# Optimization experiments

Hardware: AMD Instinct MI355X
Metric: run time of the kernel (lower is better)

Reference implementation:

```python
import jax, jax.numpy as jnp
import numpy as np

T, B, D_POSE, H, K_CODES = 30, 1024, 135, 512, 512
EPS = 1e-5


def _bn_relu(x, g, b):
    # BatchNorm1d (training-mode batch stats, biased var) + ReLU; x: (B, C, L)
    m = x.mean(axis=(0, 2), keepdims=True)
    v = x.var(axis=(0, 2), keepdims=True)
    y = g[None, :, None] * (x - m) * jax.lax.rsqrt(v + EPS) + b[None, :, None]
    return jax.nn.relu(y)


def _conv_sk(x, w):
    # Conv1d with stride == kernel_size (non-overlapping): pure reshaped GEMM.
    # x: (B, I, L), w: (O, I, K) torch layout -> (B, O, L//K)
    Bn, I, L = x.shape
    O, _, K = w.shape
    xr = x.reshape(Bn, I, L // K, K)
    return jnp.einsum('bitk,oik->bot', xr, w)


def _convT_sk(x, w):
    # ConvTranspose1d with stride == kernel_size: x (B, I, L), w (I, O, K) torch layout
    Bn, I, L = x.shape
    _, O, K = w.shape
    return jnp.einsum('bil,iok->bolk', x, w).reshape(Bn, O, L * K)


def setup_inputs() -> dict:
    key = jax.random.key(0)
    ks = jax.random.split(key, 12)
    sc = 0.05
    inp = {
        'input_seqs': jax.random.normal(ks[0], (T, B, D_POSE), jnp.float32),
        'W_in': jax.random.normal(ks[1], (D_POSE, H), jnp.float32) * sc,
        'b_in': jnp.zeros((H,), jnp.float32),
        'w_e1': jax.random.normal(ks[2], (H, H, 5), jnp.float32) * sc,
        'g_e1': jnp.ones((H,), jnp.float32), 'b_e1': jnp.zeros((H,), jnp.float32),
        'w_e2': jax.random.normal(ks[3], (H, H, 3), jnp.float32) * sc,
        'g_e2': jnp.ones((H,), jnp.float32), 'b_e2': jnp.zeros((H,), jnp.float32),
        'w_e3': jax.random.normal(ks[4], (H, H, 2), jnp.float32) * sc,
        'g_e3': jnp.ones((H,), jnp.float32), 'b_e3': jnp.zeros((H,), jnp.float32),
        'codebook': jax.random.normal(ks[5], (K_CODES, H), jnp.float32) * sc,
        'W_q': jax.random.normal(ks[6], (H, H), jnp.float32) * sc,
        'b_q': jnp.zeros((H,), jnp.float32),
        'w_d1': jax.random.normal(ks[7], (H, H, 2), jnp.float32) * sc,
        'g_d1': jnp.ones((H,), jnp.float32), 'b_d1': jnp.zeros((H,), jnp.float32),
        'w_d2': jax.random.normal(ks[8], (H, H, 3), jnp.float32) * sc,
        'g_d2': jnp.ones((H,), jnp.float32), 'b_d2': jnp.zeros((H,), jnp.float32),
        'w_d3': jax.random.normal(ks[9], (H, H, 5), jnp.float32) * sc,
        'g_d3': jnp.ones((H,), jnp.float32), 'b_d3': jnp.zeros((H,), jnp.float32),
        'W_out': jax.random.normal(ks[10], (H, D_POSE), jnp.float32) * sc,
        'b_out': jnp.zeros((D_POSE,), jnp.float32),
    }
    return inp


def reference(input_seqs, W_in, b_in, w_e1, g_e1, b_e1, w_e2, g_e2, b_e2,
              w_e3, g_e3, b_e3, codebook, W_q, b_q,
              w_d1, g_d1, b_d1, w_d2, g_d2, b_d2, w_d3, g_d3, b_d3,
              W_out, b_out):
    commitment_cost = 0.25
    # ---- EncoderCNN ----
    h = input_seqs @ W_in + b_in              # (T, B, H)
    h = jnp.transpose(h, (1, 2, 0))           # (B, H, T)
    h = _bn_relu(_conv_sk(h, w_e1), g_e1, b_e1)   # (B, H, 6)
    h = _bn_relu(_conv_sk(h, w_e2), g_e2, b_e2)   # (B, H, 2)
    z = _bn_relu(_conv_sk(h, w_e3), g_e3, b_e3)   # (B, H, 1)

    # ---- VQ (VQ_Payam, straight-through) ----
    Bn, D, L = z.shape
    flat = jnp.transpose(z, (0, 2, 1)).reshape(-1, D)            # (B*L, D)
    dist = (jnp.sum(flat ** 2, axis=1, keepdims=True)
            + jnp.sum(codebook ** 2, axis=1)
            - 2.0 * flat @ codebook.T)                           # (B*L, K)
    idx = jnp.argmin(dist, axis=1)                               # (B*L,)
    quantized = codebook[idx]                                    # (B*L, D)
    e_latent_loss = jnp.mean((jax.lax.stop_gradient(quantized) - flat) ** 2)
    q_latent_loss = jnp.mean((quantized - jax.lax.stop_gradient(flat)) ** 2)
    vq_loss = q_latent_loss + commitment_cost * e_latent_loss
    q_st = flat + jax.lax.stop_gradient(quantized - flat)        # straight-through
    avg_probs = jnp.mean(jax.nn.one_hot(idx, K_CODES, dtype=flat.dtype), axis=0)
    perplexity = jnp.exp(-jnp.sum(avg_probs * jnp.log(avg_probs + 1e-10)))

    # ---- DecoderCNN ----
    d = q_st @ W_q + b_q                      # (B, H)
    d = d[:, :, None]                         # (B, H, 1)
    d = _bn_relu(_convT_sk(d, w_d1), g_d1, b_d1)  # (B, H, 2)
    d = _bn_relu(_convT_sk(d, w_d2), g_d2, b_d2)  # (B, H, 6)
    d = _bn_relu(_convT_sk(d, w_d3), g_d3, b_d3)  # (B, H, 30)
    recon = jnp.transpose(d, (0, 2, 1)) @ W_out + b_out           # (B, T, D_POSE)
    return recon, vq_loss, perplexity
```

## Files before the change

### kernel.cpp

```cpp
#include <hip/hip_runtime.h>
#include <math.h>


typedef __attribute__((ext_vector_type(8))) short bf16x8;
typedef __attribute__((ext_vector_type(4))) float f32x4;

__device__ __forceinline__ unsigned pk_bf16(float a, float b) {
    unsigned ua = __float_as_uint(a), ub = __float_as_uint(b);
    ua += 0x7fffu + ((ua >> 16) & 1u);
    ub += 0x7fffu + ((ub >> 16) & 1u);
    return (ua >> 16) | (ub & 0xffff0000u);
}
__device__ __forceinline__ unsigned short bfh(float x) {
    unsigned u = __float_as_uint(x);
    u += 0x7fffu + ((u >> 16) & 1u);
    return (unsigned short)(u >> 16);
}
__device__ __forceinline__ float bf2f(unsigned short h) {
    return __uint_as_float(((unsigned)h) << 16);
}

template <int NV>
__device__ __forceinline__ void bn_on_raw(uint4* raw, int kbase,
                                          const float* __restrict__ bnS,
                                          const float* __restrict__ bnB) {
#pragma unroll
    for (int i = 0; i < NV; ++i) {
        unsigned* u4 = (unsigned*)&raw[i];
#pragma unroll
        for (int j = 0; j < 4; ++j) {
            const int k = kbase + (i << 3) + (j << 1);
            unsigned u = u4[j];
            float x0 = __uint_as_float(u << 16);
            float x1 = __uint_as_float(u & 0xffff0000u);
            x0 = fmaxf(fmaf(x0, bnS[k],     bnB[k]),     0.f);
            x1 = fmaxf(fmaf(x1, bnS[k + 1], bnB[k + 1]), 0.f);
            u4[j] = pk_bf16(x0, x1);
        }
    }
}

__device__ __forceinline__ void bn4(float4& a, const float* __restrict__ s,
                                    const float* __restrict__ c) {
    float4 sv = *(const float4*)s;
    float4 cv = *(const float4*)c;
    a.x = fmaxf(fmaf(a.x, sv.x, cv.x), 0.f);
    a.y = fmaxf(fmaf(a.y, sv.y, cv.y), 0.f);
    a.z = fmaxf(fmaf(a.z, sv.z, cv.z), 0.f);
    a.w = fmaxf(fmaf(a.w, sv.w, cv.w), 0.f);
}

#define FBK  32
#define FSTR 36

__global__ __launch_bounds__(256)
void k_gemm(const float* __restrict__ Abase,
            const float* __restrict__ Wt,
            float* __restrict__ Cout,
            const float* __restrict__ bnS, const float* __restrict__ bnB,
            unsigned long long* __restrict__ amin,
            const float* __restrict__ codesq,
            int Mslice, int K, int N, int decK)
{
    __shared__ __align__(16) float As[FBK][FSTR];
    __shared__ __align__(16) float Bs[FBK][FSTR];

    const int tid = threadIdx.x;
    const int z  = blockIdx.z;
    const int n0 = blockIdx.x << 5;
    const int m0 = blockIdx.y << 5;
    const int ty = tid >> 4;
    const int tx = tid & 15;

    const int a_slice = z / decK, wk = z - a_slice * decK;
    const float* Ap = Abase + (size_t)a_slice * (size_t)Mslice * (size_t)K;
    const float* Wp = Wt    + (size_t)wk * (size_t)K * (size_t)N;

    const int sr  = tid >> 3;
    const int sc4 = (tid & 7) << 2;

    int mrow = m0 + sr;
    if (mrow > Mslice - 1) mrow = Mslice - 1;
    const float* Arow_p = Ap + (size_t)mrow * K;

    float acc[2][2];
    acc[0][0] = 0.f; acc[0][1] = 0.f; acc[1][0] = 0.f; acc[1][1] = 0.f;

    float4 pa = *(const float4*)(Arow_p + sc4);
    if (bnS != nullptr) bn4(pa, bnS + sc4, bnB + sc4);
    float4 pb = *(const float4*)(Wp + (size_t)sr * N + n0 + sc4);

    for (int k0 = 0; k0 < K; k0 += FBK) {
        __syncthreads();
        As[sc4 + 0][sr] = pa.x;
        As[sc4 + 1][sr] = pa.y;
        As[sc4 + 2][sr] = pa.z;
        As[sc4 + 3][sr] = pa.w;
        *(float4*)&Bs[sr][sc4] = pb;
        const int k0n = k0 + FBK;
        if (k0n < K) {
            pa = *(const float4*)(Arow_p + k0n + sc4);
            if (bnS != nullptr) bn4(pa, bnS + k0n + sc4, bnB + k0n + sc4);
            pb = *(const float4*)(Wp + (size_t)(k0n + sr) * N + n0 + sc4);
        }
        __syncthreads();
#pragma unroll
        for (int kk = 0; kk < FBK; ++kk) {
            float2 av = *(const float2*)&As[kk][ty << 1];
            float2 bv = *(const float2*)&Bs[kk][tx << 1];
            acc[0][0] = fmaf(av.x, bv.x, acc[0][0]);
            acc[0][1] = fmaf(av.x, bv.y, acc[0][1]);
            acc[1][0] = fmaf(av.y, bv.x, acc[1][0]);
            acc[1][1] = fmaf(av.y, bv.y, acc[1][1]);
        }
    }

    if (amin != nullptr) {
        float2 cq = *(const float2*)(codesq + n0 + (tx << 1));
#pragma unroll
        for (int i = 0; i < 2; ++i) {
            const int m = m0 + (ty << 1) + i;
            float d0 = cq.x - 2.f * acc[i][0];
            float d1 = cq.y - 2.f * acc[i][1];
            int bj = (d1 < d0) ? 1 : 0;
            float best = (d1 < d0) ? d1 : d0;
            unsigned u = __float_as_uint(best);
            u = (u & 0x80000000u) ? ~u : (u | 0x80000000u);
            unsigned long long key =
                ((unsigned long long)u << 32) | (unsigned)(n0 + (tx << 1) + bj);
#pragma unroll
            for (int off = 1; off < 16; off <<= 1) {
                unsigned long long o = __shfl_xor(key, off, 64);
                if (o < key) key = o;
            }
            if (tx == 0 && m < Mslice) atomicMin(&amin[m], key);
        }
        return;
    }

#pragma unroll
    for (int i = 0; i < 2; ++i) {
        const int m = m0 + (ty << 1) + i;
        if (m < Mslice) {
            float2 v = make_float2(acc[i][0], acc[i][1]);
            *(float2*)&Cout[((size_t)z * Mslice + m) * N + n0 + (tx << 1)] = v;
        }
    }
}

#define ASTR 72

__global__ __launch_bounds__(256)
void k_mfma_b(const unsigned short* __restrict__ Abase,
              const unsigned short* __restrict__ Bt,
              unsigned short* __restrict__ Cb,
              float* __restrict__ operm,
              const float* __restrict__ bias,
              const float* __restrict__ bnS, const float* __restrict__ bnB,
              float* __restrict__ stats,
              int Mslice, int K, int N, int decK)
{
    __shared__ __align__(16) unsigned short As[128 * ASTR];
    __shared__ __align__(16) unsigned short Bs[128 * ASTR];
    __shared__ float colsum[128], colsq[128];

    const int tid  = threadIdx.x;
    const int lane = tid & 63;
    const int wave = tid >> 6;
    const int wm = (wave >> 1) << 6;
    const int wn = (wave & 1) << 6;
    const int z  = blockIdx.z;
    const int n0 = blockIdx.x << 7;
    const int m0 = blockIdx.y << 7;

    if (stats != nullptr && tid < 128) { colsum[tid] = 0.f; colsq[tid] = 0.f; }

    const int a_slice = z / decK, wk = z - a_slice * decK;
    const unsigned short* Ap = Abase + (size_t)a_slice * (size_t)Mslice * (size_t)K;
    const unsigned short* Bp = Bt + (size_t)wk * (size_t)N * (size_t)K;

    const int sr = tid >> 1;
    const int sk = (tid & 1) << 5;

    const unsigned short* Arow = Ap + (size_t)(m0 + sr) * K + sk;
    const unsigned short* Brow = Bp + (size_t)(n0 + sr) * K + sk;
    const bool bvalid = (n0 + sr) < N;

    f32x4 acc[4][4];
#pragma unroll
    for (int i = 0; i < 4; ++i)
#pragma unroll
        for (int j = 0; j < 4; ++j) acc[i][j] = (f32x4){0.f, 0.f, 0.f, 0.f};

    const int lidx = lane & 15;
    const int lq   = lane >> 4;

    uint4 pa[4], pb[4];
#pragma unroll
    for (int i = 0; i < 4; ++i) pa[i] = *(const uint4*)(Arow + (i << 3));
    if (bnS != nullptr) bn_on_raw<4>(pa, sk, bnS, bnB);
    if (bvalid) {
#pragma unroll
        for (int i = 0; i < 4; ++i) pb[i] = *(const uint4*)(Brow + (i << 3));
    } else {
#pragma unroll
        for (int i = 0; i < 4; ++i) pb[i] = make_uint4(0u, 0u, 0u, 0u);
    }

    for (int k0 = 0; k0 < K; k0 += 64) {
        __syncthreads();
        {
            uint4* dA = (uint4*)&As[sr * ASTR + sk];
            uint4* dB = (uint4*)&Bs[sr * ASTR + sk];
#pragma unroll
            for (int i = 0; i < 4; ++i) { dA[i] = pa[i]; dB[i] = pb[i]; }
        }
        const int k0n = k0 + 64;
        if (k0n < K) {
#pragma unroll
            for (int i = 0; i < 4; ++i) pa[i] = *(const uint4*)(Arow + k0n + (i << 3));
            if (bnS != nullptr) bn_on_raw<4>(pa, k0n + sk, bnS, bnB);
            if (bvalid) {
#pragma unroll
                for (int i = 0; i < 4; ++i) pb[i] = *(const uint4*)(Brow + k0n + (i << 3));
            }
        }
        __syncthreads();
#pragma unroll
        for (int ks = 0; ks < 2; ++ks) {
            const int kb = (ks << 5) + (lq << 3);
            bf16x8 af[4], bfv[4];
#pragma unroll
            for (int t = 0; t < 4; ++t)
                af[t] = *(const bf16x8*)&As[(wm + (t << 4) + lidx) * ASTR + kb];
#pragma unroll
            for (int t = 0; t < 4; ++t)
                bfv[t] = *(const bf16x8*)&Bs[(wn + (t << 4) + lidx) * ASTR + kb];
#pragma unroll
            for (int mt = 0; mt < 4; ++mt)
#pragma unroll
                for (int nt = 0; nt < 4; ++nt)
                    acc[mt][nt] = __builtin_amdgcn_mfma_f32_16x16x32_bf16(
                        af[mt], bfv[nt], acc[mt][nt], 0, 0, 0);
        }
    }

    const int rbase = lq << 2;
#pragma unroll
    for (int nt = 0; nt < 4; ++nt) {
        const int col = n0 + wn + (nt << 4) + lidx;
        const float badd = (bias != nullptr && col < N) ? bias[col] : 0.f;
        float s = 0.f, q = 0.f;
#pragma unroll
        for (int mt = 0; mt < 4; ++mt) {
#pragma unroll
            for (int r = 0; r < 4; ++r) {
                float x = acc[mt][nt][r];
                s += x; q += x * x;
                const int row = m0 + wm + (mt << 4) + rbase + r;
                if (operm != nullptr) {
                    if (col < N) {
                        const int t = row >> 10, b = row & 1023;
                        operm[(size_t)b * 4050 + t * 135 + col] = x + badd;
                    }
                } else {
                    Cb[((size_t)z * Mslice + row) * (size_t)N + col] = bfh(x + badd);
                }
            }
        }
        if (stats != nullptr) {
            s += __shfl_xor(s, 16, 64); s += __shfl_xor(s, 32, 64);
            q += __shfl_xor(q, 16, 64); q += __shfl_xor(q, 32, 64);
            if (lq == 0) {
                atomicAdd(&colsum[wn + (nt << 4) + lidx], s);
                atomicAdd(&colsq [wn + (nt << 4) + lidx], q);
            }
        }
    }
    if (stats != nullptr) {
        __syncthreads();
        if (tid < 128) {
            atomicAdd(&stats[n0 + tid],       colsum[tid]);
            atomicAdd(&stats[512 + n0 + tid], colsq[tid]);
        }
    }
}

#define BSTR 72

__global__ __launch_bounds__(256)
void k_b64(const unsigned short* __restrict__ Abase,
           const unsigned short* __restrict__ Bt,
           unsigned short* __restrict__ Cb,
           const float* __restrict__ bias,
           const float* __restrict__ bnS, const float* __restrict__ bnB,
           float* __restrict__ stats,
           int Mslice, int K, int N, int decK)
{
    __shared__ __align__(16) unsigned short As[64 * BSTR];
    __shared__ __align__(16) unsigned short Bs[64 * BSTR];
    __shared__ float colsum[64], colsq[64];

    const int tid  = threadIdx.x;
    const int lane = tid & 63;
    const int wave = tid >> 6;
    const int wm = (wave >> 1) << 5;
    const int wn = (wave & 1) << 5;
    const int z  = blockIdx.z;
    const int n0 = blockIdx.x << 6;
    const int m0 = blockIdx.y << 6;

    if (stats != nullptr && tid < 64) { colsum[tid] = 0.f; colsq[tid] = 0.f; }

    const int a_slice = z / decK, wk = z - a_slice * decK;
    const unsigned short* Ap = Abase + (size_t)a_slice * (size_t)Mslice * (size_t)K;
    const unsigned short* Bp = Bt + (size_t)wk * (size_t)N * (size_t)K;

    const int sr = tid >> 2;
    const int sk = (tid & 3) << 4;

    const unsigned short* Arow = Ap + (size_t)(m0 + sr) * K + sk;
    const unsigned short* Brow = Bp + (size_t)(n0 + sr) * K + sk;

    f32x4 acc[2][2];
#pragma unroll
    for (int i = 0; i < 2; ++i)
#pragma unroll
        for (int j = 0; j < 2; ++j) acc[i][j] = (f32x4){0.f, 0.f, 0.f, 0.f};

    const int lidx = lane & 15;
    const int lq   = lane >> 4;

    uint4 pa[2], pb[2];
    pa[0] = *(const uint4*)(Arow);
    pa[1] = *(const uint4*)(Arow + 8);
    if (bnS != nullptr) bn_on_raw<2>(pa, sk, bnS, bnB);
    pb[0] = *(const uint4*)(Brow);
    pb[1] = *(const uint4*)(Brow + 8);

    for (int k0 = 0; k0 < K; k0 += 64) {
        __syncthreads();
        {
            uint4* dA = (uint4*)&As[sr * BSTR + sk];
            uint4* dB = (uint4*)&Bs[sr * BSTR + sk];
            dA[0] = pa[0]; dA[1] = pa[1];
            dB[0] = pb[0]; dB[1] = pb[1];
        }
        const int k0n = k0 + 64;
        if (k0n < K) {
            pa[0] = *(const uint4*)(Arow + k0n);
            pa[1] = *(const uint4*)(Arow + k0n + 8);
            if (bnS != nullptr) bn_on_raw<2>(pa, k0n + sk, bnS, bnB);
            pb[0] = *(const uint4*)(Brow + k0n);
            pb[1] = *(const uint4*)(Brow + k0n + 8);
        }
        __syncthreads();
#pragma unroll
        for (int ks = 0; ks < 2; ++ks) {
            const int kb = (ks << 5) + (lq << 3);
            bf16x8 af[2], bfv[2];
#pragma unroll
            for (int t = 0; t < 2; ++t)
                af[t] = *(const bf16x8*)&As[(wm + (t << 4) + lidx) * BSTR + kb];
#pragma unroll
            for (int t = 0; t < 2; ++t)
                bfv[t] = *(const bf16x8*)&Bs[(wn + (t << 4) + lidx) * BSTR + kb];
#pragma unroll
            for (int mt = 0; mt < 2; ++mt)
#pragma unroll
                for (int nt = 0; nt < 2; ++nt)
                    acc[mt][nt] = __builtin_amdgcn_mfma_f32_16x16x32_bf16(
                        af[mt], bfv[nt], acc[mt][nt], 0, 0, 0);
        }
    }

    const int rbase = lq << 2;
#pragma unroll
    for (int nt = 0; nt < 2; ++nt) {
        const int col = n0 + wn + (nt << 4) + lidx;
        const float badd = (bias != nullptr) ? bias[col] : 0.f;
        float s = 0.f, q = 0.f;
#pragma unroll
        for (int mt = 0; mt < 2; ++mt) {
#pragma unroll
            for (int r = 0; r < 4; ++r) {
                float x = acc[mt][nt][r];
                s += x; q += x * x;
                const int row = m0 + wm + (mt << 4) + rbase + r;
                Cb[((size_t)z * Mslice + row) * (size_t)N + col] = bfh(x + badd);
            }
        }
        if (stats != nullptr) {
            s += __shfl_xor(s, 16, 64); s += __shfl_xor(s, 32, 64);
            q += __shfl_xor(q, 16, 64); q += __shfl_xor(q, 32, 64);
            if (lq == 0) {
                atomicAdd(&colsum[wn + (nt << 4) + lidx], s);
                atomicAdd(&colsq [wn + (nt << 4) + lidx], q);
            }
        }
    }
    if (stats != nullptr) {
        __syncthreads();
        if (tid < 64) {
            atomicAdd(&stats[n0 + tid],       colsum[tid]);
            atomicAdd(&stats[512 + n0 + tid], colsq[tid]);
        }
    }
}

#define S64 40

__global__ __launch_bounds__(256)
void k_sp64(const unsigned short* __restrict__ Ahg,
            const unsigned short* __restrict__ Alg,
            const unsigned short* __restrict__ Whi,
            const unsigned short* __restrict__ Wlo,
            float* __restrict__ Cout, float* __restrict__ stats,
            int Mslice, int Kp, int N, int n_terms)
{
    __shared__ __align__(16) unsigned short Ah[64 * S64];
    __shared__ __align__(16) unsigned short Al[64 * S64];
    __shared__ __align__(16) unsigned short Bh[64 * S64];
    __shared__ __align__(16) unsigned short Bl[64 * S64];
    __shared__ float colsum[64], colsq[64];

    const int tid  = threadIdx.x;
    const int lane = tid & 63;
    const int wave = tid >> 6;
    const int wm = (wave >> 1) << 5;
    const int wn = (wave & 1) << 5;
    const int z  = blockIdx.z;
    const int n0 = blockIdx.x << 6;
    const int m0 = blockIdx.y << 6;

    if (stats != nullptr && tid < 64) { colsum[tid] = 0.f; colsq[tid] = 0.f; }

    const int sr = tid >> 2;
    const int sk = (tid & 3) << 3;

    f32x4 acc[2][2];
#pragma unroll
    for (int i = 0; i < 2; ++i)
#pragma unroll
        for (int j = 0; j < 2; ++j) acc[i][j] = (f32x4){0.f, 0.f, 0.f, 0.f};

    const int lidx = lane & 15;
    const int lq   = lane >> 4;
    const int kb   = lq << 3;

    const int cpk = Kp >> 5;
    const int tot = n_terms * cpk;

    uint4 rah, ral, rbh, rblv;
    {
        const size_t ab = ((size_t)(z * n_terms) * Mslice + m0 + sr) * (size_t)Kp + sk;
        rah = *(const uint4*)(Ahg + ab);
        ral = *(const uint4*)(Alg + ab);
        const size_t bb = ((size_t)(n0 + sr)) * (size_t)Kp + sk;
        rbh = *(const uint4*)(Whi + bb);
        rblv = *(const uint4*)(Wlo + bb);
    }
    int lt = 0, lk = 32;
    if (lk >= Kp) { lk = 0; lt = 1; }

    for (int c = 0; c < tot; ++c) {
        __syncthreads();
        *(uint4*)&Ah[sr * S64 + sk] = rah;
        *(uint4*)&Al[sr * S64 + sk] = ral;
        *(uint4*)&Bh[sr * S64 + sk] = rbh;
        *(uint4*)&Bl[sr * S64 + sk] = rblv;
        if (c + 1 < tot) {
            const size_t ab = ((size_t)(z * n_terms + lt) * Mslice + m0 + sr) * (size_t)Kp + lk + sk;
            rah = *(const uint4*)(Ahg + ab);
            ral = *(const uint4*)(Alg + ab);
            const size_t bb = ((size_t)lt * N + n0 + sr) * (size_t)Kp + lk + sk;
            rbh = *(const uint4*)(Whi + bb);
            rblv = *(const uint4*)(Wlo + bb);
            lk += 32; if (lk >= Kp) { lk = 0; ++lt; }
        }
        __syncthreads();
        bf16x8 ah[2], al[2], bh[2], bl[2];
#pragma unroll
        for (int t = 0; t < 2; ++t) {
            const int ra = (wm + (t << 4) + lidx) * S64 + kb;
            ah[t] = *(const bf16x8*)&Ah[ra];
            al[t] = *(const bf16x8*)&Al[ra];
        }
#pragma unroll
        for (int t = 0; t < 2; ++t) {
            const int rb = (wn + (t << 4) + lidx) * S64 + kb;
            bh[t] = *(const bf16x8*)&Bh[rb];
            bl[t] = *(const bf16x8*)&Bl[rb];
        }
#pragma unroll
        for (int mt = 0; mt < 2; ++mt)
#pragma unroll
            for (int nt = 0; nt < 2; ++nt) {
                acc[mt][nt] = __builtin_amdgcn_mfma_f32_16x16x32_bf16(
                    ah[mt], bh[nt], acc[mt][nt], 0, 0, 0);
                acc[mt][nt] = __builtin_amdgcn_mfma_f32_16x16x32_bf16(
                    al[mt], bh[nt], acc[mt][nt], 0, 0, 0);
                acc[mt][nt] = __builtin_amdgcn_mfma_f32_16x16x32_bf16(
                    ah[mt], bl[nt], acc[mt][nt], 0, 0, 0);
            }
    }

    const int rbase = lq << 2;
#pragma unroll
    for (int nt = 0; nt < 2; ++nt) {
        const int col = n0 + wn + (nt << 4) + lidx;
        float s = 0.f, q = 0.f;
#pragma unroll
        for (int mt = 0; mt < 2; ++mt) {
#pragma unroll
            for (int r = 0; r < 4; ++r) {
                float x = acc[mt][nt][r];
                s += x; q += x * x;
                const int row = m0 + wm + (mt << 4) + rbase + r;
                Cout[((size_t)z * Mslice + row) * (size_t)N + col] = x;
            }
        }
        if (stats != nullptr) {
            s += __shfl_xor(s, 16, 64); s += __shfl_xor(s, 32, 64);
            q += __shfl_xor(q, 16, 64); q += __shfl_xor(q, 32, 64);
            if (lq == 0) {
                atomicAdd(&colsum[wn + (nt << 4) + lidx], s);
                atomicAdd(&colsq [wn + (nt << 4) + lidx], q);
            }
        }
    }
    if (stats != nullptr) {
        __syncthreads();
        if (tid < 64) {
            atomicAdd(&stats[n0 + tid],       colsum[tid]);
            atomicAdd(&stats[512 + n0 + tid], colsq[tid]);
        }
    }
}

__global__ void k_prep(float* __restrict__ zbase, unsigned long long* __restrict__ amin,
                       const float* __restrict__ codebook, float* __restrict__ codeT,
                       float* __restrict__ codesq,
                       const float* __restrict__ w_e2, unsigned short* __restrict__ whi_e2,
                       unsigned short* __restrict__ wlo_e2,
                       const float* __restrict__ w_e3, unsigned short* __restrict__ whi_e3,
                       unsigned short* __restrict__ wlo_e3,
                       const float* __restrict__ W_q,  unsigned short* __restrict__ wqb,
                       const float* __restrict__ w_d1, unsigned short* __restrict__ wd1b,
                       const float* __restrict__ w_d2, unsigned short* __restrict__ wd2b,
                       const float* __restrict__ w_d3, unsigned short* __restrict__ wd3b,
                       const float* __restrict__ W_out, unsigned short* __restrict__ woutb,
                       const float* __restrict__ in_seqs,
                       unsigned short* __restrict__ in_h, unsigned short* __restrict__ in_l)
{
    __shared__ float red[4];
    const int bid = blockIdx.x;
    const int tid = threadIdx.x;

    if (bid < 32) {
        int t = bid * 256 + tid;
        if (t < 6720) zbase[t] = 0.f;
        if (t < 1024) amin[t] = ~0ULL;
        return;
    }
    if (bid < 1056) {
        int idx = (bid - 32) * 256 + tid;
        int i = (idx >> 9) & 511, o = idx & 511;
        codeT[idx] = codebook[(o << 9) + i];
        return;
    }
    if (bid < 1568) {
        int c = bid - 1056;
        float s = 0.f;
        for (int i = tid; i < 512; i += 256) { float v = codebook[c * 512 + i]; s += v * v; }
        for (int off = 32; off; off >>= 1) s += __shfl_down(s, off, 64);
        if ((tid & 63) == 0) red[tid >> 6] = s;
        __syncthreads();
        if (tid == 0) codesq[c] = red[0] + red[1] + red[2] + red[3];
        return;
    }
    if (bid < 4640) {
        int idx = (bid - 1568) * 256 + tid;
        int i = idx & 511, o = (idx >> 9) & 511, k = idx >> 18;
        float v = w_e2[(((o << 9) + i) * 3) + k];
        unsigned short h = bfh(v);
        whi_e2[idx] = h; wlo_e2[idx] = bfh(v - bf2f(h));
        return;
    }
    if (bid < 6688) {
        int idx = (bid - 4640) * 256 + tid;
        int i = idx & 511, o = (idx >> 9) & 511, k = idx >> 18;
        float v = w_e3[(((o << 9) + i) * 2) + k];
        unsigned short h = bfh(v);
        whi_e3[idx] = h; wlo_e3[idx] = bfh(v - bf2f(h));
        return;
    }
    if (bid < 7712) {
        int idx = (bid - 6688) * 256 + tid;
        int i = idx & 511, o = (idx >> 9) & 511;
        wqb[idx] = bfh(W_q[((size_t)i << 9) + o]);
        return;
    }
    if (bid < 9760) {
        int idx = (bid - 7712) * 256 + tid;
        int i = idx & 511, o = (idx >> 9) & 511, k = idx >> 18;
        wd1b[idx] = bfh(w_d1[(((size_t)i << 9) + o) * 2 + k]);
        return;
    }
    if (bid < 12832) {
        int idx = (bid - 9760) * 256 + tid;
        int i = idx & 511, o = (idx >> 9) & 511, k = idx >> 18;
        wd2b[idx] = bfh(w_d2[(((size_t)i << 9) + o) * 3 + k]);
        return;
    }
    if (bid < 17952) {
        int idx = (bid - 12832) * 256 + tid;
        int i = idx & 511, o = (idx >> 9) & 511, k = idx >> 18;
        wd3b[idx] = bfh(w_d3[(((size_t)i << 9) + o) * 5 + k]);
        return;
    }
    if (bid < 18222) {
        int idx = (bid - 17952) * 256 + tid;
        if (idx >= 69120) return;
        int i = idx % 512, o = idx / 512;
        woutb[idx] = bfh(W_out[((size_t)i * 135) + o]);
        return;
    }
    {
        int idx = (bid - 18222) * 256 + tid;
        if (idx >= 4915200) return;
        int i = idx % 160, r = idx / 160;
        float v = (i < 135) ? in_seqs[(size_t)r * 135 + i] : 0.f;
        unsigned short h = bfh(v);
        in_h[idx] = h; in_l[idx] = bfh(v - bf2f(h));
    }
}

__global__ void k_repack(const float* __restrict__ w, float* __restrict__ wt,
                         int Kc, int total)
{
    int idx = blockIdx.x * 256 + threadIdx.x;
    if (idx >= total) return;
    int k = idx >> 18;
    int rem = idx & 262143;
    int i = rem >> 9, o = rem & 511;
    wt[idx] = w[(((o << 9) + i) * Kc + k)];
}

__global__ void k_repack_sp_weff(const float* __restrict__ weff,
                                 unsigned short* __restrict__ whi,
                                 unsigned short* __restrict__ wlo,
                                 int total)
{
    int idx = blockIdx.x * 256 + threadIdx.x;
    if (idx >= total) return;
    int i = idx % 160;
    int o = (idx / 160) & 511;
    int t = idx / 81920;
    float v = (i < 135) ? weff[((size_t)t * 135 + i) * 512 + o] : 0.f;
    unsigned short h = bfh(v);
    whi[idx] = h;
    wlo[idx] = bfh(v - bf2f(h));
}

__global__ void k_bnsplit(const float* __restrict__ x,
                          const float* __restrict__ sc, const float* __restrict__ sh,
                          unsigned short* __restrict__ hq, unsigned short* __restrict__ lq_,
                          int total4)
{
    int idx = blockIdx.x * 256 + threadIdx.x;
    if (idx >= total4) return;
    const int base = idx << 2;
    float4 f = *(const float4*)(x + base);
    const int k = base & 511;
    float4 s = *(const float4*)(sc + k);
    float4 c = *(const float4*)(sh + k);
    float y0 = fmaxf(fmaf(f.x, s.x, c.x), 0.f);
    float y1 = fmaxf(fmaf(f.y, s.y, c.y), 0.f);
    float y2 = fmaxf(fmaf(f.z, s.z, c.z), 0.f);
    float y3 = fmaxf(fmaf(f.w, s.w, c.w), 0.f);
    unsigned short h0 = bfh(y0), h1 = bfh(y1), h2 = bfh(y2), h3 = bfh(y3);
    unsigned short l0 = bfh(y0 - bf2f(h0)), l1 = bfh(y1 - bf2f(h1));
    unsigned short l2 = bfh(y2 - bf2f(h2)), l3 = bfh(y3 - bf2f(h3));
    *(uint2*)&hq[base]  = make_uint2((unsigned)h0 | ((unsigned)h1 << 16),
                                     (unsigned)h2 | ((unsigned)h3 << 16));
    *(uint2*)&lq_[base] = make_uint2((unsigned)l0 | ((unsigned)l1 << 16),
                                     (unsigned)l2 | ((unsigned)l3 << 16));
}

__global__ void k_bnapply(const unsigned short* __restrict__ x,
                          const float* __restrict__ sc, const float* __restrict__ sh,
                          unsigned short* __restrict__ y, int total8)
{
    int idx = blockIdx.x * 256 + threadIdx.x;
    if (idx >= total8) return;
    const int base = idx << 3;
    uint4 raw = *(const uint4*)(x + base);
    const int k = base & 511;
    float4 s0 = *(const float4*)(sc + k);
    float4 c0 = *(const float4*)(sh + k);
    float4 s1 = *(const float4*)(sc + k + 4);
    float4 c1 = *(const float4*)(sh + k + 4);
    unsigned* u = (unsigned*)&raw;
    float x0 = __uint_as_float(u[0] << 16),        x1 = __uint_as_float(u[0] & 0xffff0000u);
    float x2 = __uint_as_float(u[1] << 16),        x3 = __uint_as_float(u[1] & 0xffff0000u);
    float x4 = __uint_as_float(u[2] << 16),        x5 = __uint_as_float(u[2] & 0xffff0000u);
    float x6 = __uint_as_float(u[3] << 16),        x7 = __uint_as_float(u[3] & 0xffff0000u);
    x0 = fmaxf(fmaf(x0, s0.x, c0.x), 0.f); x1 = fmaxf(fmaf(x1, s0.y, c0.y), 0.f);
    x2 = fmaxf(fmaf(x2, s0.z, c0.z), 0.f); x3 = fmaxf(fmaf(x3, s0.w, c0.w), 0.f);
    x4 = fmaxf(fmaf(x4, s1.x, c1.x), 0.f); x5 = fmaxf(fmaf(x5, s1.y, c1.y), 0.f);
    x6 = fmaxf(fmaf(x6, s1.z, c1.z), 0.f); x7 = fmaxf(fmaf(x7, s1.w, c1.w), 0.f);
    *(uint4*)&y[base] = make_uint4(pk_bf16(x0, x1), pk_bf16(x2, x3),
                                   pk_bf16(x4, x5), pk_bf16(x6, x7));
}

__global__ void k_bn_fin(const float* __restrict__ stats,
                         const float* __restrict__ g, const float* __restrict__ b,
                         float* __restrict__ sc, float* __restrict__ sh, float inv_n)
{
    int c = blockIdx.x * blockDim.x + threadIdx.x;
    if (c >= 512) return;
    float m = stats[c] * inv_n;
    float v = stats[512 + c] * inv_n - m * m;
    float a = (float)((double)g[c] / sqrt((double)v + 1e-5));
    sc[c] = a;
    sh[c] = b[c] - m * a;
}

__global__ void k_vq_gather(const unsigned long long* __restrict__ amin,
                            const float* __restrict__ codebook,
                            const float* __restrict__ e3pre,
                            const float* __restrict__ sc, const float* __restrict__ sh,
                            unsigned short* __restrict__ quant_bf,
                            float* __restrict__ loss,
                            unsigned int* __restrict__ hist)
{
    int b = blockIdx.x; int t = threadIdx.x;
    unsigned int idx = (unsigned int)(amin[b] & 0xFFFFFFFFull) & 511u;
    float part = 0.f;
    for (int i = t; i < 512; i += 256) {
        float q = codebook[(size_t)idx * 512 + i];
        quant_bf[(size_t)b * 512 + i] = bfh(q);
        float x = e3pre[(size_t)b * 512 + i];
        float f = fmaxf(fmaf(x, sc[i], sh[i]), 0.f);
        float d = q - f;
        part += d * d;
    }
    for (int off = 32; off; off >>= 1) part += __shfl_down(part, off, 64);
    __shared__ float red[4];
    if ((t & 63) == 0) red[t >> 6] = part;
    __syncthreads();
    if (t == 0) {
        atomicAdd(loss, red[0] + red[1] + red[2] + red[3]);
        atomicAdd(&hist[idx], 1u);
    }
}

__global__ void k_scalars(const unsigned int* __restrict__ hist,
                          const float* __restrict__ loss, float* __restrict__ out)
{
    int t = threadIdx.x;
    float p = (float)hist[t] * (1.0f / 1024.0f);
    float e = p * logf(p + 1e-10f);
    for (int off = 32; off; off >>= 1) e += __shfl_down(e, off, 64);
    __shared__ float red[8];
    if ((t & 63) == 0) red[t >> 6] = e;
    __syncthreads();
    if (t == 0) {
        float s = 0.f;
        for (int i = 0; i < 8; ++i) s += red[i];
        out[4147200] = 1.25f * loss[0] * (1.0f / 524288.0f);
        out[4147201] = expf(-s);
    }
}

extern "C" void kernel_launch(void* const* d_in, const int* in_sizes, int n_in,
                              void* d_out, int out_size, void* d_ws, size_t ws_size,
                              hipStream_t stream)
{
    const float* in_seqs = (const float*)d_in[0];
    const float* W_in  = (const float*)d_in[1];
    const float* w_e1  = (const float*)d_in[3];
    const float* g_e1  = (const float*)d_in[4];
    const float* be1   = (const float*)d_in[5];
    const float* w_e2  = (const float*)d_in[6];
    const float* g_e2  = (const float*)d_in[7];
    const float* be2   = (const float*)d_in[8];
    const float* w_e3  = (const float*)d_in[9];
    const float* g_e3  = (const float*)d_in[10];
    const float* be3   = (const float*)d_in[11];
    const float* codebook = (const float*)d_in[12];
    const float* W_q   = (const float*)d_in[13];
    const float* b_q   = (const float*)d_in[14];
    const float* w_d1  = (const float*)d_in[15];
    const float* g_d1  = (const float*)d_in[16];
    const float* bd1   = (const float*)d_in[17];
    const float* w_d2  = (const float*)d_in[18];
    const float* g_d2  = (const float*)d_in[19];
    const float* bd2   = (const float*)d_in[20];
    const float* w_d3  = (const float*)d_in[21];
    const float* g_d3  = (const float*)d_in[22];
    const float* bd3   = (const float*)d_in[23];
    const float* W_out = (const float*)d_in[24];
    const float* b_out = (const float*)d_in[25];
    float* out = (float*)d_out;

    float* W = (float*)d_ws;
    unsigned long long* amin = (unsigned long long*)W;
    float* stats  = W + 2048;
    float* lossp  = W + 8192;
    unsigned int* hist = (unsigned int*)(W + 8256);
    float* scsh   = W + 8768;
    float* codesq = W + 14912;
    float* wt_e1  = W + 15424;
    float* weff   = W + 1326144;
    float* codeT  = W + 1671744;
    unsigned short* esw = (unsigned short*)(W + 1933888);
    unsigned short* whi_e1 = esw;
    unsigned short* wlo_e1 = esw + 409600;
    unsigned short* whi_e2 = esw + 819200;
    unsigned short* wlo_e2 = esw + 1605632;
    unsigned short* whi_e3 = esw + 2392064;
    unsigned short* wlo_e3 = esw + 2916352;
    unsigned short* in_h  = (unsigned short*)(W + 3654208);
    unsigned short* in_l  = in_h + 4915200;
    unsigned short* d3pre = (unsigned short*)(W + 3654208);
    float* e1f = W + 11518528;
    unsigned short* e1h = (unsigned short*)(W + 14664256);
    unsigned short* e1l = e1h + 3145728;
    float* e2f = W + 17809984;
    unsigned short* e2h = (unsigned short*)(W + 18858560);
    unsigned short* e2l = e2h + 1048576;
    unsigned short* d2pre = (unsigned short*)(W + 17809984);
    unsigned short* d2bf  = d2pre + 3145728;
    float* e3f = W + 20955712;
    unsigned short* quant_bf = (unsigned short*)(W + 21480000);
    unsigned short* d0bf     = (unsigned short*)(W + 21742144);
    unsigned short* d1pre    = (unsigned short*)(W + 22004288);

    unsigned short* db    = (unsigned short*)wt_e1;
    unsigned short* wqb   = db;
    unsigned short* wd1b  = db + 262144;
    unsigned short* wd2b  = db + 786432;
    unsigned short* wd3b  = db + 1572864;
    unsigned short* woutb = db + 2883584;

    float* st_e1 = stats + 0 * 1024; float* sc_e1 = scsh + 0 * 1024; float* sh_e1 = sc_e1 + 512;
    float* st_e2 = stats + 1 * 1024; float* sc_e2 = scsh + 1 * 1024; float* sh_e2 = sc_e2 + 512;
    float* st_e3 = stats + 2 * 1024; float* sc_e3 = scsh + 2 * 1024; float* sh_e3 = sc_e3 + 512;
    float* st_d1 = stats + 3 * 1024; float* sc_d1 = scsh + 3 * 1024; float* sh_d1 = sc_d1 + 512;
    float* st_d2 = stats + 4 * 1024; float* sc_d2 = scsh + 4 * 1024; float* sh_d2 = sc_d2 + 512;
    float* st_d3 = stats + 5 * 1024; float* sc_d3 = scsh + 5 * 1024; float* sh_d3 = sc_d3 + 512;

    dim3 blk(256);

    k_repack<<<dim3(5 * 1024), blk, 0, stream>>>(w_e1, wt_e1, 5, 5 * 262144);
    k_gemm<<<dim3(16, 5, 5), blk, 0, stream>>>(W_in, wt_e1, weff,
        nullptr, nullptr, nullptr, nullptr, 135, 512, 512, 5);
    k_repack_sp_weff<<<dim3(1600), blk, 0, stream>>>(weff, whi_e1, wlo_e1, 409600);

    k_prep<<<dim3(37422), blk, 0, stream>>>(stats, amin,
        codebook, codeT, codesq,
        w_e2, whi_e2, wlo_e2, w_e3, whi_e3, wlo_e3,
        W_q, wqb, w_d1, wd1b, w_d2, wd2b, w_d3, wd3b, W_out, woutb,
        in_seqs, in_h, in_l);

    k_sp64<<<dim3(8, 16, 6), blk, 0, stream>>>(in_h, in_l, whi_e1, wlo_e1,
        e1f, st_e1, 1024, 160, 512, 5);
    k_bn_fin<<<dim3(2), blk, 0, stream>>>(st_e1, g_e1, be1, sc_e1, sh_e1, 1.f / 6144.f);
    k_bnsplit<<<dim3(3072), blk, 0, stream>>>(e1f, sc_e1, sh_e1, e1h, e1l, 786432);

    k_sp64<<<dim3(8, 16, 2), blk, 0, stream>>>(e1h, e1l, whi_e2, wlo_e2,
        e2f, st_e2, 1024, 512, 512, 3);
    k_bn_fin<<<dim3(2), blk, 0, stream>>>(st_e2, g_e2, be2, sc_e2, sh_e2, 1.f / 2048.f);
    k_bnsplit<<<dim3(1024), blk, 0, stream>>>(e2f, sc_e2, sh_e2, e2h, e2l, 262144);

    k_sp64<<<dim3(8, 16, 1), blk, 0, stream>>>(e2h, e2l, whi_e3, wlo_e3,
        e3f, st_e3, 1024, 512, 512, 2);
    k_bn_fin<<<dim3(2), blk, 0, stream>>>(st_e3, g_e3, be3, sc_e3, sh_e3, 1.f / 1024.f);

    k_gemm<<<dim3(16, 32, 1), blk, 0, stream>>>(e3f, codeT, nullptr,
        sc_e3, sh_e3, amin, codesq, 1024, 512, 512, 1);
    k_vq_gather<<<dim3(1024), blk, 0, stream>>>(amin, codebook, e3f, sc_e3, sh_e3,
                                                quant_bf, lossp, hist);

    k_b64<<<dim3(8, 16, 1), blk, 0, stream>>>(quant_bf, wqb, d0bf,
        b_q, nullptr, nullptr, nullptr, 1024, 512, 512, 1);

    k_b64<<<dim3(8, 16, 2), blk, 0, stream>>>(d0bf, wd1b, d1pre,
        nullptr, nullptr, nullptr, st_d1, 1024, 512, 512, 2);
    k_bn_fin<<<dim3(2), blk, 0, stream>>>(st_d1, g_d1, bd1, sc_d1, sh_d1, 1.f / 2048.f);

    k_b64<<<dim3(8, 16, 6), blk, 0, stream>>>(d1pre, wd2b, d2pre,
        nullptr, sc_d1, sh_d1, st_d2, 1024, 512, 512, 3);
    k_bn_fin<<<dim3(2), blk, 0, stream>>>(st_d2, g_d2, bd2, sc_d2, sh_d2, 1.f / 6144.f);

    k_bnapply<<<dim3(1536), blk, 0, stream>>>(d2pre, sc_d2, sh_d2, d2bf, 393216);

    k_mfma_b<<<dim3(4, 8, 30), blk, 0, stream>>>(d2bf, wd3b, d3pre, nullptr,
        nullptr, nullptr, nullptr, st_d3, 1024, 512, 512, 5);
    k_bn_fin<<<dim3(2), blk, 0, stream>>>(st_d3, g_d3, bd3, sc_d3, sh_d3, 1.f / 30720.f);

    k_mfma_b<<<dim3(2, 240, 1), blk, 0, stream>>>(d3pre, woutb, nullptr, out,
        b_out, sc_d3, sh_d3, nullptr, 30720, 512, 135, 1);

    k_scalars<<<dim3(1), dim3(512), 0, stream>>>(hist, lossp, out);
}
```

Measured before the change: 457.3 us.

## Use direct global-to-LDS loads with XOR-swizzled tiles in several GEMM kernels

Adds new GEMM variants (k_mfma_g, k_b64g, k_sp64g) that copy tiles straight from global memory into LDS with global_load_lds. The tiles use an XOR-swizzled, unpadded layout instead of register staging into padded shared arrays, and the encoder split-precision GEMMs, the decoder q/d1 GEMMs and the d3 GEMM are switched to them. The aim is to cut register traffic and VGPR pressure on loads and avoid LDS bank conflicts without padding. In exchange, the register prefetch double-buffering of the old sp64 kernel is lost, so load latency is no longer overlapped with compute.

Result: faster. 446.5 us (-2.4%).

```diff
diff --git a/kernel.cpp b/kernel.cpp
--- a/kernel.cpp
+++ b/kernel.cpp
@@ -18,6 +18,12 @@
 }
 __device__ __forceinline__ float bf2f(unsigned short h) {
     return __uint_as_float(((unsigned)h) << 16);
+}
+
+__device__ __forceinline__ void gload16(const unsigned short* g, unsigned short* l) {
+    __builtin_amdgcn_global_load_lds(
+        (const __attribute__((address_space(1))) unsigned int*)g,
+        (__attribute__((address_space(3))) unsigned int*)l, 16, 0, 0);
 }
 
 template <int NV>
@@ -286,6 +292,332 @@
     }
 }
 
+__global__ __launch_bounds__(256)
+void k_mfma_g(const unsigned short* __restrict__ Abase,
+              const unsigned short* __restrict__ Bt,
+              unsigned short* __restrict__ Cb,
+              float* __restrict__ stats,
+              int Mslice, int K, int N, int decK)
+{
+    __shared__ __align__(16) unsigned short As[128 * 64];
+    __shared__ __align__(16) unsigned short Bs[128 * 64];
+    __shared__ float colsum[128], colsq[128];
+
+    const int tid  = threadIdx.x;
+    const int lane = tid & 63;
+    const int wave = tid >> 6;
+    const int wm = (wave >> 1) << 6;
+    const int wn = (wave & 1) << 6;
+    const int z  = blockIdx.z;
+    const int n0 = blockIdx.x << 7;
+    const int m0 = blockIdx.y << 7;
+
+    if (stats != nullptr && tid < 128) { colsum[tid] = 0.f; colsq[tid] = 0.f; }
+
+    const int a_slice = z / decK, wk = z - a_slice * decK;
+    const unsigned short* Ap = Abase + (size_t)a_slice * (size_t)Mslice * (size_t)K;
+    const unsigned short* Bp = Bt + (size_t)wk * (size_t)N * (size_t)K;
+
+    const int srow  = tid >> 3;
+    const int selem = ((tid & 7) ^ (srow & 7)) << 3;
+    const unsigned short* Asrc = Ap + (size_t)(m0 + srow) * K + selem;
+    const unsigned short* Bsrc = Bp + (size_t)(n0 + srow) * K + selem;
+    unsigned short* Adst = As + tid * 8;
+    unsigned short* Bdst = Bs + tid * 8;
+
+    f32x4 acc[4][4];
+#pragma unroll
+    for (int i = 0; i < 4; ++i)
+#pragma unroll
+        for (int j = 0; j < 4; ++j) acc[i][j] = (f32x4){0.f, 0.f, 0.f, 0.f};
+
+    const int lidx = lane & 15;
+    const int lq   = lane >> 4;
+
+    for (int k0 = 0; k0 < K; k0 += 64) {
+        __syncthreads();
+#pragma unroll
+        for (int c = 0; c < 4; ++c) {
+            gload16(Asrc + (size_t)(c << 5) * K + k0, Adst + (c << 11));
+            gload16(Bsrc + (size_t)(c << 5) * K + k0, Bdst + (c << 11));
+        }
+        __syncthreads();
+#pragma unroll
+        for (int ks = 0; ks < 2; ++ks) {
+            const int ub = (ks << 2) + lq;
+            const int uo = (ub ^ (lidx & 7)) << 3;
+            bf16x8 af[4], bfv[4];
+#pragma unroll
+            for (int t = 0; t < 4; ++t)
+                af[t] = *(const bf16x8*)&As[((wm + (t << 4) + lidx) << 6) + uo];
+#pragma unroll
+            for (int t = 0; t < 4; ++t)
+                bfv[t] = *(const bf16x8*)&Bs[((wn + (t << 4) + lidx) << 6) + uo];
+#pragma unroll
+            for (int mt = 0; mt < 4; ++mt)
+#pragma unroll
+                for (int nt = 0; nt < 4; ++nt)
+                    acc[mt][nt] = __builtin_amdgcn_mfma_f32_16x16x32_bf16(
+                        af[mt], bfv[nt], acc[mt][nt], 0, 0, 0);
+        }
+    }
+
+    const int rbase = lq << 2;
+#pragma unroll
+    for (int nt = 0; nt < 4; ++nt) {
+        const int col = n0 + wn + (nt << 4) + lidx;
+        float s = 0.f, q = 0.f;
+#pragma unroll
+        for (int mt = 0; mt < 4; ++mt) {
+#pragma unroll
+            for (int r = 0; r < 4; ++r) {
+                float x = acc[mt][nt][r];
+                s += x; q += x * x;
+                const int row = m0 + wm + (mt << 4) + rbase + r;
+                Cb[((size_t)z * Mslice + row) * (size_t)N + col] = bfh(x);
+            }
+        }
+        if (stats != nullptr) {
+            s += __shfl_xor(s, 16, 64); s += __shfl_xor(s, 32, 64);
+            q += __shfl_xor(q, 16, 64); q += __shfl_xor(q, 32, 64);
+            if (lq == 0) {
+                atomicAdd(&colsum[wn + (nt << 4) + lidx], s);
+                atomicAdd(&colsq [wn + (nt << 4) + lidx], q);
+            }
+        }
+    }
+    if (stats != nullptr) {
+        __syncthreads();
+        if (tid < 128) {
+            atomicAdd(&stats[n0 + tid],       colsum[tid]);
+            atomicAdd(&stats[512 + n0 + tid], colsq[tid]);
+        }
+    }
+}
+
+__global__ __launch_bounds__(256)
+void k_b64g(const unsigned short* __restrict__ Abase,
+            const unsigned short* __restrict__ Bt,
+            unsigned short* __restrict__ Cb,
+            const float* __restrict__ bias,
+            float* __restrict__ stats,
+            int Mslice, int K, int N, int decK)
+{
+    __shared__ __align__(16) unsigned short As[64 * 64];
+    __shared__ __align__(16) unsigned short Bs[64 * 64];
+    __shared__ float colsum[64], colsq[64];
+
+    const int tid  = threadIdx.x;
+    const int lane = tid & 63;
+    const int wave = tid >> 6;
+    const int wm = (wave >> 1) << 5;
+    const int wn = (wave & 1) << 5;
+    const int z  = blockIdx.z;
+    const int n0 = blockIdx.x << 6;
+    const int m0 = blockIdx.y << 6;
+
+    if (stats != nullptr && tid < 64) { colsum[tid] = 0.f; colsq[tid] = 0.f; }
+
+    const int a_slice = z / decK, wk = z - a_slice * decK;
+    const unsigned short* Ap = Abase + (size_t)a_slice * (size_t)Mslice * (size_t)K;
+    const unsigned short* Bp = Bt + (size_t)wk * (size_t)N * (size_t)K;
+
+    const int srow  = tid >> 3;
+    const int selem = ((tid & 7) ^ (srow & 7)) << 3;
+    const unsigned short* Asrc = Ap + (size_t)(m0 + srow) * K + selem;
+    const unsigned short* Bsrc = Bp + (size_t)(n0 + srow) * K + selem;
+    unsigned short* Adst = As + tid * 8;
+    unsigned short* Bdst = Bs + tid * 8;
+
+    f32x4 acc[2][2];
+#pragma unroll
+    for (int i = 0; i < 2; ++i)
+#pragma unroll
+        for (int j = 0; j < 2; ++j) acc[i][j] = (f32x4){0.f, 0.f, 0.f, 0.f};
+
+    const int lidx = lane & 15;
+    const int lq   = lane >> 4;
+
+    for (int k0 = 0; k0 < K; k0 += 64) {
+        __syncthreads();
+#pragma unroll
+        for (int c = 0; c < 2; ++c) {
+            gload16(Asrc + (size_t)(c << 5) * K + k0, Adst + (c << 11));
+            gload16(Bsrc + (size_t)(c << 5) * K + k0, Bdst + (c << 11));
+        }
+        __syncthreads();
+#pragma unroll
+        for (int ks = 0; ks < 2; ++ks) {
+            const int ub = (ks << 2) + lq;
+            const int uo = (ub ^ (lidx & 7)) << 3;
+            bf16x8 af[2], bfv[2];
+#pragma unroll
+            for (int t = 0; t < 2; ++t)
+                af[t] = *(const bf16x8*)&As[((wm + (t << 4) + lidx) << 6) + uo];
+#pragma unroll
+            for (int t = 0; t < 2; ++t)
+                bfv[t] = *(const bf16x8*)&Bs[((wn + (t << 4) + lidx) << 6) + uo];
+#pragma unroll
+            for (int mt = 0; mt < 2; ++mt)
+#pragma unroll
+                for (int nt = 0; nt < 2; ++nt)
+                    acc[mt][nt] = __builtin_amdgcn_mfma_f32_16x16x32_bf16(
+                        af[mt], bfv[nt], acc[mt][nt], 0, 0, 0);
+        }
+    }
+
+    const int rbase = lq << 2;
+#pragma unroll
+    for (int nt = 0; nt < 2; ++nt) {
+        const int col = n0 + wn + (nt << 4) + lidx;
+        const float badd = (bias != nullptr) ? bias[col] : 0.f;
+        float s = 0.f, q = 0.f;
+#pragma unroll
+        for (int mt = 0; mt < 2; ++mt) {
+#pragma unroll
+            for (int r = 0; r < 4; ++r) {
+                float x = acc[mt][nt][r];
+                s += x; q += x * x;
+                const int row = m0 + wm + (mt << 4) + rbase + r;
+                Cb[((size_t)z * Mslice + row) * (size_t)N + col] = bfh(x + badd);
+            }
+        }
+        if (stats != nullptr) {
+            s += __shfl_xor(s, 16, 64); s += __shfl_xor(s, 32, 64);
+            q += __shfl_xor(q, 16, 64); q += __shfl_xor(q, 32, 64);
+            if (lq == 0) {
+                atomicAdd(&colsum[wn + (nt << 4) + lidx], s);
+                atomicAdd(&colsq [wn + (nt << 4) + lidx], q);
+            }
+        }
+    }
+    if (stats != nullptr) {
+        __syncthreads();
+        if (tid < 64) {
+            atomicAdd(&stats[n0 + tid],       colsum[tid]);
+            atomicAdd(&stats[512 + n0 + tid], colsq[tid]);
+        }
+    }
+}
+
+__global__ __launch_bounds__(256)
+void k_sp64g(const unsigned short* __restrict__ Ahg,
+             const unsigned short* __restrict__ Alg,
+             const unsigned short* __restrict__ Whi,
+             const unsigned short* __restrict__ Wlo,
+             float* __restrict__ Cout, float* __restrict__ stats,
+             int Mslice, int Kp, int N, int n_terms)
+{
+    __shared__ __align__(16) unsigned short Ah[64 * 32];
+    __shared__ __align__(16) unsigned short Al[64 * 32];
+    __shared__ __align__(16) unsigned short Bh[64 * 32];
+    __shared__ __align__(16) unsigned short Bl[64 * 32];
+    __shared__ float colsum[64], colsq[64];
+
+    const int tid  = threadIdx.x;
+    const int lane = tid & 63;
+    const int wave = tid >> 6;
+    const int wm = (wave >> 1) << 5;
+    const int wn = (wave & 1) << 5;
+    const int z  = blockIdx.z;
+    const int n0 = blockIdx.x << 6;
+    const int m0 = blockIdx.y << 6;
+
+    if (stats != nullptr && tid < 64) { colsum[tid] = 0.f; colsq[tid] = 0.f; }
+
+    const int srow  = tid >> 2;
+    const int selem = ((tid & 3) ^ (srow & 3)) << 3;
+    unsigned short* Ahd = Ah + tid * 8;
+    unsigned short* Ald = Al + tid * 8;
+    unsigned short* Bhd = Bh + tid * 8;
+    unsigned short* Bld = Bl + tid * 8;
+
+    f32x4 acc[2][2];
+#pragma unroll
+    for (int i = 0; i < 2; ++i)
+#pragma unroll
+        for (int j = 0; j < 2; ++j) acc[i][j] = (f32x4){0.f, 0.f, 0.f, 0.f};
+
+    const int lidx = lane & 15;
+    const int lq   = lane >> 4;
+    const int uo   = (lq ^ (lidx & 3)) << 3;
+
+    const int cpk = Kp >> 5;
+    const int tot = n_terms * cpk;
+
+    int lt = 0, lk = 0;
+    for (int c = 0; c < tot; ++c) {
+        __syncthreads();
+        {
+            const size_t ab = ((size_t)(z * n_terms + lt) * Mslice + m0 + srow)
+                              * (size_t)Kp + lk + selem;
+            const size_t bb = ((size_t)lt * N + n0 + srow) * (size_t)Kp + lk + selem;
+            gload16(Ahg + ab, Ahd);
+            gload16(Alg + ab, Ald);
+            gload16(Whi + bb, Bhd);
+            gload16(Wlo + bb, Bld);
+        }
+        lk += 32; if (lk >= Kp) { lk = 0; ++lt; }
+        __syncthreads();
+        bf16x8 ah[2], al[2], bh[2], bl[2];
+#pragma unroll
+        for (int t = 0; t < 2; ++t) {
+            const int ra = ((wm + (t << 4) + lidx) << 5) + uo;
+            ah[t] = *(const bf16x8*)&Ah[ra];
+            al[t] = *(const bf16x8*)&Al[ra];
+        }
+#pragma unroll
+        for (int t = 0; t < 2; ++t) {
+            const int rb = ((wn + (t << 4) + lidx) << 5) + uo;
+            bh[t] = *(const bf16x8*)&Bh[rb];
+            bl[t] = *(const bf16x8*)&Bl[rb];
+        }
+#pragma unroll
+        for (int mt = 0; mt < 2; ++mt)
+#pragma unroll
+            for (int nt = 0; nt < 2; ++nt) {
+                acc[mt][nt] = __builtin_amdgcn_mfma_f32_16x16x32_bf16(
+                    ah[mt], bh[nt], acc[mt][nt], 0, 0, 0);
+                acc[mt][nt] = __builtin_amdgcn_mfma_f32_16x16x32_bf16(
+                    al[mt], bh[nt], acc[mt][nt], 0, 0, 0);
+                acc[mt][nt] = __builtin_amdgcn_mfma_f32_16x16x32_bf16(
+                    ah[mt], bl[nt], acc[mt][nt], 0, 0, 0);
+            }
+    }
+
+    const int rbase = lq << 2;
+#pragma unroll
+    for (int nt = 0; nt < 2; ++nt) {
+        const int col = n0 + wn + (nt << 4) + lidx;
+        float s = 0.f, q = 0.f;
+#pragma unroll
+        for (int mt = 0; mt < 2; ++mt) {
+#pragma unroll
+            for (int r = 0; r < 4; ++r) {
+                float x = acc[mt][nt][r];
+                s += x; q += x * x;
+                const int row = m0 + wm + (mt << 4) + rbase + r;
+                Cout[((size_t)z * Mslice + row) * (size_t)N + col] = x;
+            }
+        }
+        if (stats != nullptr) {
+            s += __shfl_xor(s, 16, 64); s += __shfl_xor(s, 32, 64);
+            q += __shfl_xor(q, 16, 64); q += __shfl_xor(q, 32, 64);
+            if (lq == 0) {
+                atomicAdd(&colsum[wn + (nt << 4) + lidx], s);
+                atomicAdd(&colsq [wn + (nt << 4) + lidx], q);
+            }
+        }
+    }
+    if (stats != nullptr) {
+        __syncthreads();
+        if (tid < 64) {
+            atomicAdd(&stats[n0 + tid],       colsum[tid]);
+            atomicAdd(&stats[512 + n0 + tid], colsq[tid]);
+        }
+    }
+}
+
 #define BSTR 72
 
 __global__ __launch_bounds__(256)
@@ -388,136 +720,6 @@
                 s += x; q += x * x;
                 const int row = m0 + wm + (mt << 4) + rbase + r;
                 Cb[((size_t)z * Mslice + row) * (size_t)N + col] = bfh(x + badd);
-            }
-        }
-        if (stats != nullptr) {
-            s += __shfl_xor(s, 16, 64); s += __shfl_xor(s, 32, 64);
-            q += __shfl_xor(q, 16, 64); q += __shfl_xor(q, 32, 64);
-            if (lq == 0) {
-                atomicAdd(&colsum[wn + (nt << 4) + lidx], s);
-                atomicAdd(&colsq [wn + (nt << 4) + lidx], q);
-            }
-        }
-    }
-    if (stats != nullptr) {
-        __syncthreads();
-        if (tid < 64) {
-            atomicAdd(&stats[n0 + tid],       colsum[tid]);
-            atomicAdd(&stats[512 + n0 + tid], colsq[tid]);
-        }
-    }
-}
-
-#define S64 40
-
-__global__ __launch_bounds__(256)
-void k_sp64(const unsigned short* __restrict__ Ahg,
-            const unsigned short* __restrict__ Alg,
-            const unsigned short* __restrict__ Whi,
-            const unsigned short* __restrict__ Wlo,
-            float* __restrict__ Cout, float* __restrict__ stats,
-            int Mslice, int Kp, int N, int n_terms)
-{
-    __shared__ __align__(16) unsigned short Ah[64 * S64];
-    __shared__ __align__(16) unsigned short Al[64 * S64];
-    __shared__ __align__(16) unsigned short Bh[64 * S64];
-    __shared__ __align__(16) unsigned short Bl[64 * S64];
-    __shared__ float colsum[64], colsq[64];
-
-    const int tid  = threadIdx.x;
-    const int lane = tid & 63;
-    const int wave = tid >> 6;
-    const int wm = (wave >> 1) << 5;
-    const int wn = (wave & 1) << 5;
-    const int z  = blockIdx.z;
-    const int n0 = blockIdx.x << 6;
-    const int m0 = blockIdx.y << 6;
-
-    if (stats != nullptr && tid < 64) { colsum[tid] = 0.f; colsq[tid] = 0.f; }
-
-    const int sr = tid >> 2;
-    const int sk = (tid & 3) << 3;
-
-    f32x4 acc[2][2];
-#pragma unroll
-    for (int i = 0; i < 2; ++i)
-#pragma unroll
-        for (int j = 0; j < 2; ++j) acc[i][j] = (f32x4){0.f, 0.f, 0.f, 0.f};
-
-    const int lidx = lane & 15;
-    const int lq   = lane >> 4;
-    const int kb   = lq << 3;
-
-    const int cpk = Kp >> 5;
-    const int tot = n_terms * cpk;
-
-    uint4 rah, ral, rbh, rblv;
-    {
-        const size_t ab = ((size_t)(z * n_terms) * Mslice + m0 + sr) * (size_t)Kp + sk;
-        rah = *(const uint4*)(Ahg + ab);
-        ral = *(const uint4*)(Alg + ab);
-        const size_t bb = ((size_t)(n0 + sr)) * (size_t)Kp + sk;
-        rbh = *(const uint4*)(Whi + bb);
-        rblv = *(const uint4*)(Wlo + bb);
-    }
-    int lt = 0, lk = 32;
-    if (lk >= Kp) { lk = 0; lt = 1; }
-
-    for (int c = 0; c < tot; ++c) {
-        __syncthreads();
-        *(uint4*)&Ah[sr * S64 + sk] = rah;
-        *(uint4*)&Al[sr * S64 + sk] = ral;
-        *(uint4*)&Bh[sr * S64 + sk] = rbh;
-        *(uint4*)&Bl[sr * S64 + sk] = rblv;
-        if (c + 1 < tot) {
-            const size_t ab = ((size_t)(z * n_terms + lt) * Mslice + m0 + sr) * (size_t)Kp + lk + sk;
-            rah = *(const uint4*)(Ahg + ab);
-            ral = *(const uint4*)(Alg + ab);
-            const size_t bb = ((size_t)lt * N + n0 + sr) * (size_t)Kp + lk + sk;
-            rbh = *(const uint4*)(Whi + bb);
-            rblv = *(const uint4*)(Wlo + bb);
-            lk += 32; if (lk >= Kp) { lk = 0; ++lt; }
-        }
-        __syncthreads();
-        bf16x8 ah[2], al[2], bh[2], bl[2];
-#pragma unroll
-        for (int t = 0; t < 2; ++t) {
-            const int ra = (wm + (t << 4) + lidx) * S64 + kb;
-            ah[t] = *(const bf16x8*)&Ah[ra];
-            al[t] = *(const bf16x8*)&Al[ra];
-        }
-#pragma unroll
-        for (int t = 0; t < 2; ++t) {
-            const int rb = (wn + (t << 4) + lidx) * S64 + kb;
-            bh[t] = *(const bf16x8*)&Bh[rb];
-            bl[t] = *(const bf16x8*)&Bl[rb];
-        }
-#pragma unroll
-        for (int mt = 0; mt < 2; ++mt)
-#pragma unroll
-            for (int nt = 0; nt < 2; ++nt) {
-                acc[mt][nt] = __builtin_amdgcn_mfma_f32_16x16x32_bf16(
-                    ah[mt], bh[nt], acc[mt][nt], 0, 0, 0);
-                acc[mt][nt] = __builtin_amdgcn_mfma_f32_16x16x32_bf16(
-                    al[mt], bh[nt], acc[mt][nt], 0, 0, 0);
-                acc[mt][nt] = __builtin_amdgcn_mfma_f32_16x16x32_bf16(
-                    ah[mt], bl[nt], acc[mt][nt], 0, 0, 0);
-            }
-    }
-
-    const int rbase = lq << 2;
-#pragma unroll
-    for (int nt = 0; nt < 2; ++nt) {
-        const int col = n0 + wn + (nt << 4) + lidx;
-        float s = 0.f, q = 0.f;
-#pragma unroll
-        for (int mt = 0; mt < 2; ++mt) {
-#pragma unroll
-            for (int r = 0; r < 4; ++r) {
-                float x = acc[mt][nt][r];
-                s += x; q += x * x;
-                const int row = m0 + wm + (mt << 4) + rbase + r;
-                Cout[((size_t)z * Mslice + row) * (size_t)N + col] = x;
             }
         }
         if (stats != nullptr) {
@@ -865,17 +1067,17 @@
         W_q, wqb, w_d1, wd1b, w_d2, wd2b, w_d3, wd3b, W_out, woutb,
         in_seqs, in_h, in_l);
 
-    k_sp64<<<dim3(8, 16, 6), blk, 0, stream>>>(in_h, in_l, whi_e1, wlo_e1,
+    k_sp64g<<<dim3(8, 16, 6), blk, 0, stream>>>(in_h, in_l, whi_e1, wlo_e1,
         e1f, st_e1, 1024, 160, 512, 5);
     k_bn_fin<<<dim3(2), blk, 0, stream>>>(st_e1, g_e1, be1, sc_e1, sh_e1, 1.f / 6144.f);
     k_bnsplit<<<dim3(3072), blk, 0, stream>>>(e1f, sc_e1, sh_e1, e1h, e1l, 786432);
 
-    k_sp64<<<dim3(8, 16, 2), blk, 0, stream>>>(e1h, e1l, whi_e2, wlo_e2,
+    k_sp64g<<<dim3(8, 16, 2), blk, 0, stream>>>(e1h, e1l, whi_e2, wlo_e2,
         e2f, st_e2, 1024, 512, 512, 3);
     k_bn_fin<<<dim3(2), blk, 0, stream>>>(st_e2, g_e2, be2, sc_e2, sh_e2, 1.f / 2048.f);
     k_bnsplit<<<dim3(1024), blk, 0, stream>>>(e2f, sc_e2, sh_e2, e2h, e2l, 262144);
 
-    k_sp64<<<dim3(8, 16, 1), blk, 0, stream>>>(e2h, e2l, whi_e3, wlo_e3,
+    k_sp64g<<<dim3(8, 16, 1), blk, 0, stream>>>(e2h, e2l, whi_e3, wlo_e3,
         e3f, st_e3, 1024, 512, 512, 2);
     k_bn_fin<<<dim3(2), blk, 0, stream>>>(st_e3, g_e3, be3, sc_e3, sh_e3, 1.f / 1024.f);
 
@@ -884,11 +1086,11 @@
     k_vq_gather<<<dim3(1024), blk, 0, stream>>>(amin, codebook, e3f, sc_e3, sh_e3,
                                                 quant_bf, lossp, hist);
 
-    k_b64<<<dim3(8, 16, 1), blk, 0, stream>>>(quant_bf, wqb, d0bf,
-        b_q, nullptr, nullptr, nullptr, 1024, 512, 512, 1);
-
-    k_b64<<<dim3(8, 16, 2), blk, 0, stream>>>(d0bf, wd1b, d1pre,
-        nullptr, nullptr, nullptr, st_d1, 1024, 512, 512, 2);
+    k_b64g<<<dim3(8, 16, 1), blk, 0, stream>>>(quant_bf, wqb, d0bf,
+        b_q, nullptr, 1024, 512, 512, 1);
+
+    k_b64g<<<dim3(8, 16, 2), blk, 0, stream>>>(d0bf, wd1b, d1pre,
+        nullptr, st_d1, 1024, 512, 512, 2);
     k_bn_fin<<<dim3(2), blk, 0, stream>>>(st_d1, g_d1, bd1, sc_d1, sh_d1, 1.f / 2048.f);
 
     k_b64<<<dim3(8, 16, 6), blk, 0, stream>>>(d1pre, wd2b, d2pre,
@@ -897,8 +1099,8 @@
 
     k_bnapply<<<dim3(1536), blk, 0, stream>>>(d2pre, sc_d2, sh_d2, d2bf, 393216);
 
-    k_mfma_b<<<dim3(4, 8, 30), blk, 0, stream>>>(d2bf, wd3b, d3pre, nullptr,
-        nullptr, nullptr, nullptr, st_d3, 1024, 512, 512, 5);
+    k_mfma_g<<<dim3(4, 8, 30), blk, 0, stream>>>(d2bf, wd3b, d3pre,
+        st_d3, 1024, 512, 512, 5);
     k_bn_fin<<<dim3(2), blk, 0, stream>>>(st_d3, g_d3, bd3, sc_d3, sh_d3, 1.f / 30720.f);
 
     k_mfma_b<<<dim3(2, 240, 1), blk, 0, stream>>>(d3pre, woutb, nullptr, out,
```
